# Optimization experiments

Measured on AMD Instinct MI355X. Metric: run time of the kernel, lower is better.

## Reference

```python
import jax, jax.numpy as jnp
import numpy as np

N_NODES = 98304
N_GRAPHS = 2048
NODES_PER_GRAPH = 48
N_EDGES = 393216
NODE_IN = 128
EMB = 64
HID = 256
N_LAYERS = 6
ATTN_DIM = 256
N_HEADS = 4
HEAD_DIM = ATTN_DIM // N_HEADS
OUT_DIM = 1024


def setup_inputs() -> dict:
    key = jax.random.key(0)
    ks = iter(jax.random.split(key, 40))

    def nrm(shape, fan_in):
        return (jax.random.normal(next(ks), shape, dtype=jnp.float32)
                / np.float32(np.sqrt(fan_in)))

    x = jax.random.normal(next(ks), (N_NODES, NODE_IN), dtype=jnp.float32)
    edge_index = jax.random.randint(next(ks), (2, N_EDGES), 0, N_NODES, dtype=jnp.int32)
    batch = (jnp.arange(N_NODES, dtype=jnp.int32) // NODES_PER_GRAPH)

    inp = {
        "x": x,
        "edge_index": edge_index,
        "batch": batch,
        "W_embed": nrm((NODE_IN, EMB), NODE_IN),
        "b_embed": jnp.zeros((EMB,), jnp.float32),
        "W1": nrm((N_LAYERS, EMB, HID), EMB),
        "b1": jnp.zeros((N_LAYERS, HID), jnp.float32),
        "W2": nrm((N_LAYERS, HID, 2 * HID), HID),
        "b2": jnp.zeros((N_LAYERS, 2 * HID), jnp.float32),
        "W3": nrm((N_LAYERS, 2 * HID, EMB), 2 * HID),
        "b3": jnp.zeros((N_LAYERS, EMB), jnp.float32),
        "Wp": nrm((EMB, ATTN_DIM), EMB),
        "bp": jnp.zeros((ATTN_DIM,), jnp.float32),
        "q": jax.random.normal(next(ks), (1, ATTN_DIM), dtype=jnp.float32),
        "W_in": nrm((ATTN_DIM, 3 * ATTN_DIM), ATTN_DIM),
        "b_in": jnp.zeros((3 * ATTN_DIM,), jnp.float32),
        "W_out": nrm((ATTN_DIM, ATTN_DIM), ATTN_DIM),
        "b_out": jnp.zeros((ATTN_DIM,), jnp.float32),
        "Wh1": nrm((ATTN_DIM, HID), ATTN_DIM),
        "bh1": jnp.zeros((HID,), jnp.float32),
        "ln_g": jnp.ones((HID,), jnp.float32),
        "ln_b": jnp.zeros((HID,), jnp.float32),
        "Wh2": nrm((HID, OUT_DIM), HID),
        "bh2": jnp.zeros((OUT_DIM,), jnp.float32),
    }
    return inp


def _forward(x, edge_index, batch, W_embed, b_embed, W1, b1, W2, b2, W3, b3,
             Wp, bp, q, W_in, b_in, W_out, b_out, Wh1, bh1, ln_g, ln_b, Wh2, bh2):
    row = edge_index[0]  # only row is used, matching the torch module

    # node embed
    h = x @ W_embed + b_embed  # [N, 64]

    # 6 GNN layers: gather h[row] -> 3-layer MLP -> scatter_add back to row
    for l in range(N_LAYERS):
        m = jax.nn.relu(h[row] @ W1[l] + b1[l])          # [E, 256]
        m = jax.nn.relu(m @ W2[l] + b2[l])               # [E, 512]
        dh = m @ W3[l] + b3[l]                           # [E, 64]
        h = h + jax.ops.segment_sum(dh, row, num_segments=N_NODES)

    # attention pooling per graph (single learned query, 4 heads)
    hp = h @ Wp + bp                                     # [N, 256]
    Wq, Wk, Wv = W_in[:, :ATTN_DIM], W_in[:, ATTN_DIM:2 * ATTN_DIM], W_in[:, 2 * ATTN_DIM:]
    bq, bk, bv = b_in[:ATTN_DIM], b_in[ATTN_DIM:2 * ATTN_DIM], b_in[2 * ATTN_DIM:]

    qh = ((q @ Wq + bq).reshape(N_HEADS, HEAD_DIM)
          / jnp.asarray(np.sqrt(HEAD_DIM), jnp.float32))  # [H, D]
    k = (hp @ Wk + bk).reshape(N_NODES, N_HEADS, HEAD_DIM)
    v = (hp @ Wv + bv).reshape(N_NODES, N_HEADS, HEAD_DIM)

    scores = jnp.einsum('nhd,hd->nh', k, qh)             # [N, H]
    smax = jax.ops.segment_max(scores, batch, num_segments=N_GRAPHS)  # [B, H]
    e = jnp.exp(scores - smax[batch])
    denom = jax.ops.segment_sum(e, batch, num_segments=N_GRAPHS)      # [B, H]
    w = e / denom[batch]                                  # [N, H]
    pooled = jax.ops.segment_sum(w[:, :, None] * v, batch, num_segments=N_GRAPHS)  # [B, H, D]
    attn = pooled.reshape(N_GRAPHS, ATTN_DIM) @ W_out + b_out  # [B, 256]

    # projection head: ReLU -> Linear -> ReLU -> LayerNorm -> Linear
    t = jax.nn.relu(attn) @ Wh1 + bh1
    t = jax.nn.relu(t)
    mu = jnp.mean(t, axis=-1, keepdims=True)
    var = jnp.mean((t - mu) ** 2, axis=-1, keepdims=True)
    t = (t - mu) * jax.lax.rsqrt(var + 1e-5) * ln_g + ln_b
    return t @ Wh2 + bh2                                  # [B, 1024]


def reference(x, edge_index, batch, W_embed, b_embed, W1, b1, W2, b2, W3, b3,
              Wp, bp, q, W_in, b_in, W_out, b_out, Wh1, bh1, ln_g, ln_b, Wh2, bh2):
    return _forward(x, edge_index, batch, W_embed, b_embed, W1, b1, W2, b2, W3, b3,
                    Wp, bp, q, W_in, b_in, W_out, b_out, Wh1, bh1, ln_g, ln_b, Wh2, bh2)
```

## Files before the change

### kernel.cpp

```cpp
#include <hip/hip_runtime.h>
#include <hip/hip_bf16.h>

#define N_NODES 98304
#define N_GRAPHS 2048
#define N_EDGES 393216
#define EMB 64
#define HID 256
#define N_LAYERS_ 6

typedef __attribute__((ext_vector_type(8))) short short8v;
typedef __attribute__((ext_vector_type(4))) float f32x4;
#define MFMA16(a, b, c) __builtin_amdgcn_mfma_f32_16x16x32_bf16(a, b, c, 0, 0, 0)

__device__ __forceinline__ unsigned short f2bf(float x) {
    unsigned int u = __float_as_uint(x);
    u = (u + 0x7fffu + ((u >> 16) & 1u)) >> 16;
    return (unsigned short)u;
}
__device__ __forceinline__ float bf2f(unsigned short h) {
    return __uint_as_float(((unsigned int)h) << 16);
}
__device__ __forceinline__ int swz(int row, int col, int rowc) {
    return (row * rowc + col) ^ ((row & 7) << 3);
}

__global__ __launch_bounds__(256) void zero_cnt_kernel(int* __restrict__ cnt) {
    int i = blockIdx.x * 256 + threadIdx.x;
    if (i < N_NODES) cnt[i] = 0;
}
__global__ __launch_bounds__(256) void hist_kernel(const int* __restrict__ row,
                                                   int* __restrict__ cnt) {
    int i = blockIdx.x * 256 + threadIdx.x;
    if (i < N_EDGES) atomicAdd(&cnt[row[i]], 1);
}

__global__ __launch_bounds__(64) void prep_frag_kernel(
    const float* __restrict__ W, unsigned short* __restrict__ oh,
    unsigned short* __restrict__ ol, int K, int N)
{
    const int NF = N >> 4, KS = K >> 5;
    const int fpl = NF * KS;
    const int layer = blockIdx.x / fpl;
    const int fid = blockIdx.x % fpl;
    const int nf = fid / KS, ks = fid % KS;
    const int lane = threadIdx.x;
    const float* Wl = W + (size_t)layer * K * N;
    const int n = nf * 16 + (lane & 15);
    const int kb = ks * 32 + (lane >> 4) * 8;
    short8v vh, vl;
    #pragma unroll
    for (int j = 0; j < 8; j++) {
        float wv = Wl[(size_t)(kb + j) * N + n];
        unsigned short hi = f2bf(wv);
        vh[j] = (short)hi;
        vl[j] = (short)f2bf(wv - bf2f(hi));
    }
    size_t o = (size_t)layer * K * N + ((size_t)(nf * KS + ks) * 64 + lane) * 8;
    *reinterpret_cast<short8v*>(oh + o) = vh;
    *reinterpret_cast<short8v*>(ol + o) = vl;
}

__global__ __launch_bounds__(256) void embed_mfma_kernel(
    const float* __restrict__ x,
    const unsigned short* __restrict__ Weh, const unsigned short* __restrict__ Wel,
    const float* __restrict__ b, float* __restrict__ h)
{
    __shared__ __attribute__((aligned(16))) unsigned short xh[32 * 128];
    __shared__ __attribute__((aligned(16))) unsigned short xl[32 * 128];
    const int tid = threadIdx.x;
    const int lane = tid & 63, w = tid >> 6;
    const int lm = lane & 15, lq = lane >> 4;
    const int base = blockIdx.x * 32;
    {
        int row = tid >> 3, c0 = (tid & 7) * 16;
        const float4* p = reinterpret_cast<const float4*>(x + (size_t)(base + row) * 128 + c0);
        float4 u0 = p[0], u1 = p[1], u2 = p[2], u3 = p[3];
        float vals[16] = {u0.x,u0.y,u0.z,u0.w, u1.x,u1.y,u1.z,u1.w,
                          u2.x,u2.y,u2.z,u2.w, u3.x,u3.y,u3.z,u3.w};
        short8v vh0, vl0, vh1, vl1;
        #pragma unroll
        for (int j = 0; j < 8; j++) {
            unsigned short hi = f2bf(vals[j]);
            vh0[j] = (short)hi; vl0[j] = (short)f2bf(vals[j] - bf2f(hi));
            unsigned short hi1 = f2bf(vals[8 + j]);
            vh1[j] = (short)hi1; vl1[j] = (short)f2bf(vals[8 + j] - bf2f(hi1));
        }
        *reinterpret_cast<short8v*>(&xh[swz(row, c0, 128)]) = vh0;
        *reinterpret_cast<short8v*>(&xl[swz(row, c0, 128)]) = vl0;
        *reinterpret_cast<short8v*>(&xh[swz(row, c0 + 8, 128)]) = vh1;
        *reinterpret_cast<short8v*>(&xl[swz(row, c0 + 8, 128)]) = vl1;
    }
    __syncthreads();
    f32x4 acc0, acc1;
    {
        float bv = b[w * 16 + lm];
        acc0 = f32x4{bv, bv, bv, bv};
        acc1 = acc0;
    }
    #pragma unroll
    for (int ks = 0; ks < 4; ks++) {
        short8v a0h = *reinterpret_cast<const short8v*>(&xh[swz(lm, ks * 32 + lq * 8, 128)]);
        short8v a0l = *reinterpret_cast<const short8v*>(&xl[swz(lm, ks * 32 + lq * 8, 128)]);
        short8v a1h = *reinterpret_cast<const short8v*>(&xh[swz(16 + lm, ks * 32 + lq * 8, 128)]);
        short8v a1l = *reinterpret_cast<const short8v*>(&xl[swz(16 + lm, ks * 32 + lq * 8, 128)]);
        size_t bi = ((size_t)(w * 4 + ks) * 64 + lane) * 8;
        short8v bh = *reinterpret_cast<const short8v*>(Weh + bi);
        short8v bl = *reinterpret_cast<const short8v*>(Wel + bi);
        acc0 = MFMA16(a0h, bh, acc0); acc0 = MFMA16(a0l, bh, acc0); acc0 = MFMA16(a0h, bl, acc0);
        acc1 = MFMA16(a1h, bh, acc1); acc1 = MFMA16(a1l, bh, acc1); acc1 = MFMA16(a1h, bl, acc1);
    }
    #pragma unroll
    for (int r = 0; r < 4; r++) {
        h[(size_t)(base + lq * 4 + r) * 64 + w * 16 + lm] = acc0[r];
        h[(size_t)(base + 16 + lq * 4 + r) * 64 + w * 16 + lm] = acc1[r];
    }
}

__global__ __launch_bounds__(512, 4) void layer_mfma_kernel(
    float* __restrict__ h, const int* __restrict__ cnt,
    const unsigned short* __restrict__ W1h, const unsigned short* __restrict__ W1l,
    const float* __restrict__ b1,
    const unsigned short* __restrict__ W2h, const unsigned short* __restrict__ W2l,
    const float* __restrict__ b2,
    const unsigned short* __restrict__ W3h, const unsigned short* __restrict__ W3l,
    const float* __restrict__ b3)
{
    __shared__ __attribute__((aligned(16))) unsigned short hsh[32 * 64];
    __shared__ __attribute__((aligned(16))) unsigned short hsl[32 * 64];
    __shared__ __attribute__((aligned(16))) unsigned short m1h_[32 * 256];
    __shared__ __attribute__((aligned(16))) unsigned short m1l_[32 * 256];
    __shared__ __attribute__((aligned(16))) unsigned short m2h_[32 * 256];
    __shared__ __attribute__((aligned(16))) unsigned short m2l_[32 * 256];
    const int tid = threadIdx.x;
    const int lane = tid & 63, w = tid >> 6;
    const int lm = lane & 15, lq = lane >> 4;
    const int base = blockIdx.x * 32;

    {
        int row = tid >> 4, c0 = (tid & 15) * 4;
        const float4 u = *reinterpret_cast<const float4*>(h + (size_t)(base + row) * 64 + c0);
        float vals[4] = {u.x, u.y, u.z, u.w};
        unsigned short vh[4], vl[4];
        #pragma unroll
        for (int j = 0; j < 4; j++) {
            vh[j] = f2bf(vals[j]);
            vl[j] = f2bf(vals[j] - bf2f(vh[j]));
        }
        int idx = swz(row, c0, 64);
        *reinterpret_cast<uint2*>(&hsh[idx]) = *reinterpret_cast<uint2*>(vh);
        *reinterpret_cast<uint2*>(&hsl[idx]) = *reinterpret_cast<uint2*>(vl);
    }
    __syncthreads();

    {
        f32x4 acc[2][2];
        #pragma unroll
        for (int f = 0; f < 2; f++) {
            float bv = b1[(2 * w + f) * 16 + lm];
            acc[f][0] = f32x4{bv, bv, bv, bv};
            acc[f][1] = acc[f][0];
        }
        #pragma unroll
        for (int ks = 0; ks < 2; ks++) {
            short8v ah0 = *reinterpret_cast<const short8v*>(&hsh[swz(lm, ks * 32 + lq * 8, 64)]);
            short8v al0 = *reinterpret_cast<const short8v*>(&hsl[swz(lm, ks * 32 + lq * 8, 64)]);
            short8v ah1 = *reinterpret_cast<const short8v*>(&hsh[swz(16 + lm, ks * 32 + lq * 8, 64)]);
            short8v al1 = *reinterpret_cast<const short8v*>(&hsl[swz(16 + lm, ks * 32 + lq * 8, 64)]);
            #pragma unroll
            for (int f = 0; f < 2; f++) {
                size_t bi = ((size_t)((2 * w + f) * 2 + ks) * 64 + lane) * 8;
                short8v bh = *reinterpret_cast<const short8v*>(W1h + bi);
                short8v bl = *reinterpret_cast<const short8v*>(W1l + bi);
                acc[f][0] = MFMA16(ah0, bh, acc[f][0]);
                acc[f][0] = MFMA16(al0, bh, acc[f][0]);
                acc[f][0] = MFMA16(ah0, bl, acc[f][0]);
                acc[f][1] = MFMA16(ah1, bh, acc[f][1]);
                acc[f][1] = MFMA16(al1, bh, acc[f][1]);
                acc[f][1] = MFMA16(ah1, bl, acc[f][1]);
            }
        }
        #pragma unroll
        for (int f = 0; f < 2; f++)
            #pragma unroll
            for (int m = 0; m < 2; m++)
                #pragma unroll
                for (int r = 0; r < 4; r++) {
                    int row = m * 16 + lq * 4 + r;
                    int col = (2 * w + f) * 16 + lm;
                    float v = fmaxf(acc[f][m][r], 0.f);
                    unsigned short hi = f2bf(v);
                    m1h_[swz(row, col, 256)] = hi;
                    m1l_[swz(row, col, 256)] = f2bf(v - bf2f(hi));
                }
    }
    __syncthreads();

    const int nfc = w & 3, kq = w >> 2;
    f32x4 dacc[2];
    if (kq == 0) {
        float bv = b3[nfc * 16 + lm];
        dacc[0] = f32x4{bv, bv, bv, bv};
    } else {
        dacc[0] = f32x4{0.f, 0.f, 0.f, 0.f};
    }
    dacc[1] = dacc[0];

    #pragma unroll
    for (int c = 0; c < 2; ++c) {
        {
            f32x4 acc[2][2];
            #pragma unroll
            for (int f = 0; f < 2; f++) {
                float bv = b2[(c * 16 + 2 * w + f) * 16 + lm];
                acc[f][0] = f32x4{bv, bv, bv, bv};
                acc[f][1] = acc[f][0];
            }
            #pragma unroll
            for (int ks = 0; ks < 8; ks++) {
                short8v ah0 = *reinterpret_cast<const short8v*>(&m1h_[swz(lm, ks * 32 + lq * 8, 256)]);
                short8v al0 = *reinterpret_cast<const short8v*>(&m1l_[swz(lm, ks * 32 + lq * 8, 256)]);
                short8v ah1 = *reinterpret_cast<const short8v*>(&m1h_[swz(16 + lm, ks * 32 + lq * 8, 256)]);
                short8v al1 = *reinterpret_cast<const short8v*>(&m1l_[swz(16 + lm, ks * 32 + lq * 8, 256)]);
                #pragma unroll
                for (int f = 0; f < 2; f++) {
                    size_t bi = ((size_t)((c * 16 + 2 * w + f) * 8 + ks) * 64 + lane) * 8;
                    short8v bh = *reinterpret_cast<const short8v*>(W2h + bi);
                    short8v bl = *reinterpret_cast<const short8v*>(W2l + bi);
                    acc[f][0] = MFMA16(ah0, bh, acc[f][0]);
                    acc[f][0] = MFMA16(al0, bh, acc[f][0]);
                    acc[f][0] = MFMA16(ah0, bl, acc[f][0]);
                    acc[f][1] = MFMA16(ah1, bh, acc[f][1]);
                    acc[f][1] = MFMA16(al1, bh, acc[f][1]);
                    acc[f][1] = MFMA16(ah1, bl, acc[f][1]);
                }
            }
            #pragma unroll
            for (int f = 0; f < 2; f++)
                #pragma unroll
                for (int m = 0; m < 2; m++)
                    #pragma unroll
                    for (int r = 0; r < 4; r++) {
                        int row = m * 16 + lq * 4 + r;
                        int col = (2 * w + f) * 16 + lm;
                        float v = fmaxf(acc[f][m][r], 0.f);
                        unsigned short hi = f2bf(v);
                        m2h_[swz(row, col, 256)] = hi;
                        m2l_[swz(row, col, 256)] = f2bf(v - bf2f(hi));
                    }
        }
        __syncthreads();
        {
            #pragma unroll
            for (int kl = 0; kl < 4; kl++) {
                int ksl = kq * 4 + kl;
                short8v ah0 = *reinterpret_cast<const short8v*>(&m2h_[swz(lm, ksl * 32 + lq * 8, 256)]);
                short8v al0 = *reinterpret_cast<const short8v*>(&m2l_[swz(lm, ksl * 32 + lq * 8, 256)]);
                short8v ah1 = *reinterpret_cast<const short8v*>(&m2h_[swz(16 + lm, ksl * 32 + lq * 8, 256)]);
                short8v al1 = *reinterpret_cast<const short8v*>(&m2l_[swz(16 + lm, ksl * 32 + lq * 8, 256)]);
                int ksg = c * 8 + ksl;
                size_t bi = ((size_t)(nfc * 16 + ksg) * 64 + lane) * 8;
                short8v bh = *reinterpret_cast<const short8v*>(W3h + bi);
                short8v bl = *reinterpret_cast<const short8v*>(W3l + bi);
                dacc[0] = MFMA16(ah0, bh, dacc[0]);
                dacc[0] = MFMA16(al0, bh, dacc[0]);
                dacc[0] = MFMA16(ah0, bl, dacc[0]);
                dacc[1] = MFMA16(ah1, bh, dacc[1]);
                dacc[1] = MFMA16(al1, bh, dacc[1]);
                dacc[1] = MFMA16(ah1, bl, dacc[1]);
            }
        }
        __syncthreads();
    }

    float* scr = reinterpret_cast<float*>(m1h_);
    if (kq == 1) {
        #pragma unroll
        for (int m = 0; m < 2; m++)
            #pragma unroll
            for (int r = 0; r < 4; r++)
                scr[(m * 16 + lq * 4 + r) * 64 + nfc * 16 + lm] = dacc[m][r];
    }
    __syncthreads();
    if (kq == 0) {
        #pragma unroll
        for (int m = 0; m < 2; m++)
            #pragma unroll
            for (int r = 0; r < 4; r++) {
                int rr = base + m * 16 + lq * 4 + r;
                float dv = dacc[m][r] + scr[(m * 16 + lq * 4 + r) * 64 + nfc * 16 + lm];
                size_t gi = (size_t)rr * 64 + nfc * 16 + lm;
                h[gi] = h[gi] + (float)cnt[rr] * dv;
            }
    }
}

__global__ __launch_bounds__(256) void prec_kernel(
    const float* __restrict__ q, const float* __restrict__ W_in,
    const float* __restrict__ b_in, const float* __restrict__ Wp,
    const float* __restrict__ bp, float* __restrict__ prec)
{
    __shared__ float qh_s[256];
    __shared__ float u_s[4 * 256];
    const int tid = threadIdx.x;
    {
        float acc = b_in[tid];
        for (int j = 0; j < 256; j++) acc += q[j] * W_in[j * 768 + tid];
        qh_s[tid] = acc * 0.125f;
    }
    __syncthreads();
    {
        #pragma unroll
        for (int hd = 0; hd < 4; hd++) {
            float a = 0.f;
            for (int d = 0; d < 64; d++)
                a += W_in[tid * 768 + 256 + hd * 64 + d] * qh_s[hd * 64 + d];
            u_s[hd * 256 + tid] = a;
        }
    }
    __syncthreads();
    {
        int hd = tid >> 6, i = tid & 63;
        float a = 0.f;
        for (int j = 0; j < 256; j++) a += Wp[i * 256 + j] * u_s[hd * 256 + j];
        prec[hd * 64 + i] = a;
    }
    if (tid < 4) {
        float a = 0.f;
        for (int j = 0; j < 256; j++) a += bp[j] * u_s[tid * 256 + j];
        for (int d = 0; d < 64; d++) a += b_in[256 + tid * 64 + d] * qh_s[tid * 64 + d];
        prec[256 + tid] = a;
    }
}

__global__ __launch_bounds__(64) void attnpool_kernel(
    const float* __restrict__ h, const float* __restrict__ prec,
    float* __restrict__ hw)
{
    __shared__ float hs[48 * 65];
    __shared__ float ss[4 * 64];
    __shared__ float ds_[4];
    __shared__ float wl[48 * 4];
    const int lane = threadIdx.x;
    const int g = blockIdx.x;
    #pragma unroll
    for (int hd = 0; hd < 4; hd++) ss[hd * 64 + lane] = prec[hd * 64 + lane];
    if (lane < 4) ds_[lane] = prec[256 + lane];
    for (int r = 0; r < 48; r++)
        hs[r * 65 + lane] = h[((size_t)g * 48 + r) * 64 + lane];
    __syncthreads();
    float sc[4] = {0.f, 0.f, 0.f, 0.f};
    if (lane < 48) {
        #pragma unroll
        for (int hd = 0; hd < 4; hd++) sc[hd] = ds_[hd];
        for (int c = 0; c < 64; c++) {
            float a = hs[lane * 65 + c];
            #pragma unroll
            for (int hd = 0; hd < 4; hd++) sc[hd] += a * ss[hd * 64 + c];
        }
    }
    #pragma unroll
    for (int hd = 0; hd < 4; hd++) {
        float v = (lane < 48) ? sc[hd] : -3.0e38f;
        #pragma unroll
        for (int m = 32; m >= 1; m >>= 1) v = fmaxf(v, __shfl_xor(v, m, 64));
        float e = (lane < 48) ? __expf(sc[hd] - v) : 0.f;
        float s = e;
        #pragma unroll
        for (int m = 32; m >= 1; m >>= 1) s += __shfl_xor(s, m, 64);
        if (lane < 48) wl[lane * 4 + hd] = e / s;
    }
    __syncthreads();
    float acc[4] = {0.f, 0.f, 0.f, 0.f};
    for (int n = 0; n < 48; n++) {
        float hv = hs[n * 65 + lane];
        #pragma unroll
        for (int hd = 0; hd < 4; hd++) acc[hd] += wl[n * 4 + hd] * hv;
    }
    #pragma unroll
    for (int hd = 0; hd < 4; hd++) hw[(size_t)g * 256 + hd * 64 + lane] = acc[hd];
}

__global__ __launch_bounds__(256) void tail_kernel(
    const float* __restrict__ hw,
    const float* __restrict__ Wp, const float* __restrict__ bp,
    const float* __restrict__ W_in, const float* __restrict__ b_in,
    const float* __restrict__ W_out, const float* __restrict__ b_out,
    const float* __restrict__ Wh1, const float* __restrict__ bh1,
    const float* __restrict__ ln_g, const float* __restrict__ ln_b,
    const float* __restrict__ Wh2, const float* __restrict__ bh2,
    float* __restrict__ out)
{
    __shared__ float hw_s[8 * 256];
    __shared__ float hpw_s[8 * 1024];
    __shared__ float pooled_s[8 * 256];
    __shared__ float attn_s[8 * 256];
    __shared__ float t_s[8 * 256];
    __shared__ float mu_s[8], rs_s[8];
    const int tid = threadIdx.x;
    const int g0 = blockIdx.x * 8;
    #pragma unroll
    for (int r = 0; r < 8; r++)
        hw_s[r * 256 + tid] = hw[(size_t)g0 * 256 + r * 256 + tid];
    __syncthreads();
    {
        float acc[8][4];
        #pragma unroll
        for (int g = 0; g < 8; g++)
            #pragma unroll
            for (int hd = 0; hd < 4; hd++) acc[g][hd] = 0.f;
        for (int i = 0; i < 64; i++) {
            float wv = Wp[i * 256 + tid];
            #pragma unroll
            for (int g = 0; g < 8; g++)
                #pragma unroll
                for (int hd = 0; hd < 4; hd++)
                    acc[g][hd] += hw_s[g * 256 + hd * 64 + i] * wv;
        }
        float bpj = bp[tid];
        #pragma unroll
        for (int g = 0; g < 8; g++)
            #pragma unroll
            for (int hd = 0; hd < 4; hd++)
                hpw_s[g * 1024 + hd * 256 + tid] = acc[g][hd] + bpj;
    }
    __syncthreads();
    {
        const int hd = tid >> 6;
        float acc[8];
        #pragma unroll
        for (int g = 0; g < 8; g++) acc[g] = 0.f;
        for (int j = 0; j < 256; j++) {
            float wv = W_in[j * 768 + 512 + tid];
            #pragma unroll
            for (int g = 0; g < 8; g++)
                acc[g] += hpw_s[g * 1024 + hd * 256 + j] * wv;
        }
        float bb = b_in[512 + tid];
        #pragma unroll
        for (int g = 0; g < 8; g++) pooled_s[g * 256 + tid] = acc[g] + bb;
    }
    __syncthreads();
    {
        float acc[8];
        #pragma unroll
        for (int g = 0; g < 8; g++) acc[g] = 0.f;
        for (int j = 0; j < 256; j++) {
            float wv = W_out[j * 256 + tid];
            #pragma unroll
            for (int g = 0; g < 8; g++) acc[g] += pooled_s[g * 256 + j] * wv;
        }
        float bb = b_out[tid];
        #pragma unroll
        for (int g = 0; g < 8; g++)
            attn_s[g * 256 + tid] = fmaxf(acc[g] + bb, 0.f);
    }
    __syncthreads();
    {
        float acc[8];
        #pragma unroll
        for (int g = 0; g < 8; g++) acc[g] = 0.f;
        for (int j = 0; j < 256; j++) {
            float wv = Wh1[j * 256 + tid];
            #pragma unroll
            for (int g = 0; g < 8; g++) acc[g] += attn_s[g * 256 + j] * wv;
        }
        float bb = bh1[tid];
        #pragma unroll
        for (int g = 0; g < 8; g++)
            t_s[g * 256 + tid] = fmaxf(acc[g] + bb, 0.f);
    }
    __syncthreads();
    if (tid < 8) {
        float s = 0.f;
        for (int c = 0; c < 256; c++) s += t_s[tid * 256 + c];
        float mu = s * (1.f / 256.f);
        float v = 0.f;
        for (int c = 0; c < 256; c++) {
            float d = t_s[tid * 256 + c] - mu;
            v += d * d;
        }
        v *= (1.f / 256.f);
        mu_s[tid] = mu;
        rs_s[tid] = rsqrtf(v + 1e-5f);
    }
    __syncthreads();
    {
        float gg = ln_g[tid], bb = ln_b[tid];
        #pragma unroll
        for (int r = 0; r < 8; r++)
            t_s[r * 256 + tid] = (t_s[r * 256 + tid] - mu_s[r]) * rs_s[r] * gg + bb;
    }
    __syncthreads();
    {
        float acc[8][4];
        float4 bb = *reinterpret_cast<const float4*>(bh2 + tid * 4);
        #pragma unroll
        for (int g = 0; g < 8; g++) {
            acc[g][0] = bb.x; acc[g][1] = bb.y; acc[g][2] = bb.z; acc[g][3] = bb.w;
        }
        for (int j = 0; j < 256; j++) {
            float4 wv = *reinterpret_cast<const float4*>(Wh2 + (size_t)j * 1024 + tid * 4);
            #pragma unroll
            for (int g = 0; g < 8; g++) {
                float tv = t_s[g * 256 + j];
                acc[g][0] += tv * wv.x; acc[g][1] += tv * wv.y;
                acc[g][2] += tv * wv.z; acc[g][3] += tv * wv.w;
            }
        }
        #pragma unroll
        for (int g = 0; g < 8; g++)
            *reinterpret_cast<float4*>(out + (size_t)(g0 + g) * 1024 + tid * 4) =
                make_float4(acc[g][0], acc[g][1], acc[g][2], acc[g][3]);
    }
}

extern "C" void kernel_launch(void* const* d_in, const int* in_sizes, int n_in,
                              void* d_out, int out_size, void* d_ws, size_t ws_size,
                              hipStream_t stream) {
    const float* x       = (const float*)d_in[0];
    const int*   edge    = (const int*)d_in[1];
    const float* W_embed = (const float*)d_in[3];
    const float* b_embed = (const float*)d_in[4];
    const float* W1 = (const float*)d_in[5];
    const float* b1 = (const float*)d_in[6];
    const float* W2 = (const float*)d_in[7];
    const float* b2 = (const float*)d_in[8];
    const float* W3 = (const float*)d_in[9];
    const float* b3 = (const float*)d_in[10];
    const float* Wp = (const float*)d_in[11];
    const float* bp = (const float*)d_in[12];
    const float* q  = (const float*)d_in[13];
    const float* W_in  = (const float*)d_in[14];
    const float* b_in  = (const float*)d_in[15];
    const float* W_out = (const float*)d_in[16];
    const float* b_out = (const float*)d_in[17];
    const float* Wh1 = (const float*)d_in[18];
    const float* bh1 = (const float*)d_in[19];
    const float* ln_g = (const float*)d_in[20];
    const float* ln_b = (const float*)d_in[21];
    const float* Wh2 = (const float*)d_in[22];
    const float* bh2 = (const float*)d_in[23];
    float* out = (float*)d_out;

    char* ws = (char*)d_ws;
    int*   cnt  = (int*)(ws + 0);
    float* h    = (float*)(ws + 393216);
    float* hw   = (float*)(ws + 25559040);
    float* prec = (float*)(ws + 27656192);
    unsigned short* W1h = (unsigned short*)(ws + 27657232);
    unsigned short* W1l = (unsigned short*)(ws + 27853840);
    unsigned short* W2h = (unsigned short*)(ws + 28050448);
    unsigned short* W2l = (unsigned short*)(ws + 29623312);
    unsigned short* W3h = (unsigned short*)(ws + 31196176);
    unsigned short* W3l = (unsigned short*)(ws + 31589392);
    unsigned short* Weh = (unsigned short*)(ws + 31982608);
    unsigned short* Wel = (unsigned short*)(ws + 31998992);

    zero_cnt_kernel<<<N_NODES / 256, 256, 0, stream>>>(cnt);
    hist_kernel<<<N_EDGES / 256, 256, 0, stream>>>(edge, cnt);

    prep_frag_kernel<<<1 * (64 / 16) * (128 / 32), 64, 0, stream>>>(W_embed, Weh, Wel, 128, 64);
    prep_frag_kernel<<<6 * (256 / 16) * (64 / 32), 64, 0, stream>>>(W1, W1h, W1l, 64, 256);
    prep_frag_kernel<<<6 * (512 / 16) * (256 / 32), 64, 0, stream>>>(W2, W2h, W2l, 256, 512);
    prep_frag_kernel<<<6 * (64 / 16) * (512 / 32), 64, 0, stream>>>(W3, W3h, W3l, 512, 64);

    embed_mfma_kernel<<<N_NODES / 32, 256, 0, stream>>>(x, Weh, Wel, b_embed, h);
    for (int l = 0; l < N_LAYERS_; l++) {
        layer_mfma_kernel<<<N_NODES / 32, 512, 0, stream>>>(
            h, cnt,
            W1h + (size_t)l * EMB * HID,     W1l + (size_t)l * EMB * HID,     b1 + (size_t)l * HID,
            W2h + (size_t)l * HID * 2 * HID, W2l + (size_t)l * HID * 2 * HID, b2 + (size_t)l * 2 * HID,
            W3h + (size_t)l * 2 * HID * EMB, W3l + (size_t)l * 2 * HID * EMB, b3 + (size_t)l * EMB);
    }
    prec_kernel<<<1, 256, 0, stream>>>(q, W_in, b_in, Wp, bp, prec);
    attnpool_kernel<<<N_GRAPHS, 64, 0, stream>>>(h, prec, hw);
    tail_kernel<<<N_GRAPHS / 8, 256, 0, stream>>>(hw, Wp, bp, W_in, b_in,
                                                  W_out, b_out, Wh1, bh1,
                                                  ln_g, ln_b, Wh2, bh2, out);
}
```

Measured before the change: 918.7 us.

## Fold Wp into V projection and run tail MLP on split-bf16 MFMA

Precomputes a block-diagonal matrix that folds the Wp projection and the value slice of W_in into one 256x256 operator plus bias, which removes one GEMM stage from the tail. The tail then runs every dense stage (G, W_out, Wh1, Wh2) on 3-pass split-bf16 MFMA over 32-graph tiles, with the intermediates kept in swizzled LDS. LayerNorm is parallelised with shuffle reductions. The cost is extra weight-prep launches and a small change in numerics from the hi/lo bf16 split.

```diff
diff --git a/kernel.cpp b/kernel.cpp
--- a/kernel.cpp
+++ b/kernel.cpp
@@ -58,6 +58,27 @@
     size_t o = (size_t)layer * K * N + ((size_t)(nf * KS + ks) * 64 + lane) * 8;
     *reinterpret_cast<short8v*>(oh + o) = vh;
     *reinterpret_cast<short8v*>(ol + o) = vl;
+}
+
+__global__ __launch_bounds__(256) void gbuild_kernel(
+    const float* __restrict__ Wp, const float* __restrict__ bp,
+    const float* __restrict__ W_in, const float* __restrict__ b_in,
+    float* __restrict__ Gm, float* __restrict__ Gd)
+{
+    const int idx = blockIdx.x * 256 + threadIdx.x;
+    const int q = idx >> 8, p = idx & 255;
+    float s = 0.f;
+    if ((q >> 6) == (p >> 6)) {
+        const float* wr = Wp + (q & 63) * 256;
+        for (int j = 0; j < 256; j++) s += wr[j] * W_in[j * 768 + 512 + p];
+    }
+    Gm[q * 256 + p] = s;
+    if (blockIdx.x == 0) {
+        const int pp = threadIdx.x;
+        float dsum = b_in[512 + pp];
+        for (int j = 0; j < 256; j++) dsum += bp[j] * W_in[j * 768 + 512 + pp];
+        Gd[pp] = dsum;
+    }
 }
 
 __global__ __launch_bounds__(256) void embed_mfma_kernel(
@@ -380,137 +401,173 @@
     for (int hd = 0; hd < 4; hd++) hw[(size_t)g * 256 + hd * 64 + lane] = acc[hd];
 }
 
-__global__ __launch_bounds__(256) void tail_kernel(
+__device__ __forceinline__ void tail_stage(
+    const unsigned short* __restrict__ inh, const unsigned short* __restrict__ inl,
+    const unsigned short* __restrict__ wh, const unsigned short* __restrict__ wl,
+    const float* __restrict__ bias, const bool do_relu,
+    unsigned short* __restrict__ oth, unsigned short* __restrict__ otl,
+    float* __restrict__ tf32,
+    const int w, const int lane, const int lm, const int lq)
+{
+    f32x4 acc[2][2];
+    #pragma unroll
+    for (int f = 0; f < 2; f++) {
+        float bv = bias[(2 * w + f) * 16 + lm];
+        acc[f][0] = f32x4{bv, bv, bv, bv};
+        acc[f][1] = acc[f][0];
+    }
+    #pragma unroll
+    for (int ks = 0; ks < 8; ks++) {
+        short8v ah0 = *reinterpret_cast<const short8v*>(&inh[swz(lm, ks * 32 + lq * 8, 256)]);
+        short8v al0 = *reinterpret_cast<const short8v*>(&inl[swz(lm, ks * 32 + lq * 8, 256)]);
+        short8v ah1 = *reinterpret_cast<const short8v*>(&inh[swz(16 + lm, ks * 32 + lq * 8, 256)]);
+        short8v al1 = *reinterpret_cast<const short8v*>(&inl[swz(16 + lm, ks * 32 + lq * 8, 256)]);
+        #pragma unroll
+        for (int f = 0; f < 2; f++) {
+            size_t bi = ((size_t)((2 * w + f) * 8 + ks) * 64 + lane) * 8;
+            short8v bh = *reinterpret_cast<const short8v*>(wh + bi);
+            short8v bl = *reinterpret_cast<const short8v*>(wl + bi);
+            acc[f][0] = MFMA16(ah0, bh, acc[f][0]);
+            acc[f][0] = MFMA16(al0, bh, acc[f][0]);
+            acc[f][0] = MFMA16(ah0, bl, acc[f][0]);
+            acc[f][1] = MFMA16(ah1, bh, acc[f][1]);
+            acc[f][1] = MFMA16(al1, bh, acc[f][1]);
+            acc[f][1] = MFMA16(ah1, bl, acc[f][1]);
+        }
+    }
+    #pragma unroll
+    for (int f = 0; f < 2; f++)
+        #pragma unroll
+        for (int m = 0; m < 2; m++)
+            #pragma unroll
+            for (int r = 0; r < 4; r++) {
+                int row = m * 16 + lq * 4 + r;
+                int col = (2 * w + f) * 16 + lm;
+                float v = acc[f][m][r];
+                if (do_relu) v = fmaxf(v, 0.f);
+                if (tf32) {
+                    tf32[row * 256 + col] = v;
+                } else {
+                    unsigned short hi = f2bf(v);
+                    oth[swz(row, col, 256)] = hi;
+                    otl[swz(row, col, 256)] = f2bf(v - bf2f(hi));
+                }
+            }
+}
+
+__global__ __launch_bounds__(512, 4) void tail_mfma_kernel(
     const float* __restrict__ hw,
-    const float* __restrict__ Wp, const float* __restrict__ bp,
-    const float* __restrict__ W_in, const float* __restrict__ b_in,
-    const float* __restrict__ W_out, const float* __restrict__ b_out,
-    const float* __restrict__ Wh1, const float* __restrict__ bh1,
+    const unsigned short* __restrict__ Gh, const unsigned short* __restrict__ Gl,
+    const float* __restrict__ Gd,
+    const unsigned short* __restrict__ Woh, const unsigned short* __restrict__ Wol,
+    const float* __restrict__ b_out,
+    const unsigned short* __restrict__ Wh1h, const unsigned short* __restrict__ Wh1l,
+    const float* __restrict__ bh1,
     const float* __restrict__ ln_g, const float* __restrict__ ln_b,
-    const float* __restrict__ Wh2, const float* __restrict__ bh2,
+    const unsigned short* __restrict__ Wh2h, const unsigned short* __restrict__ Wh2l,
+    const float* __restrict__ bh2,
     float* __restrict__ out)
 {
-    __shared__ float hw_s[8 * 256];
-    __shared__ float hpw_s[8 * 1024];
-    __shared__ float pooled_s[8 * 256];
-    __shared__ float attn_s[8 * 256];
-    __shared__ float t_s[8 * 256];
-    __shared__ float mu_s[8], rs_s[8];
+    __shared__ __attribute__((aligned(16))) unsigned short L[32768];
+    unsigned short* Ah = L;
+    unsigned short* Al = L + 8192;
+    unsigned short* Bh = L + 16384;
+    unsigned short* Bl = L + 24576;
+    float* tf = reinterpret_cast<float*>(L + 16384);
     const int tid = threadIdx.x;
-    const int g0 = blockIdx.x * 8;
-    #pragma unroll
-    for (int r = 0; r < 8; r++)
-        hw_s[r * 256 + tid] = hw[(size_t)g0 * 256 + r * 256 + tid];
-    __syncthreads();
-    {
-        float acc[8][4];
-        #pragma unroll
-        for (int g = 0; g < 8; g++)
-            #pragma unroll
-            for (int hd = 0; hd < 4; hd++) acc[g][hd] = 0.f;
-        for (int i = 0; i < 64; i++) {
-            float wv = Wp[i * 256 + tid];
-            #pragma unroll
-            for (int g = 0; g < 8; g++)
-                #pragma unroll
-                for (int hd = 0; hd < 4; hd++)
-                    acc[g][hd] += hw_s[g * 256 + hd * 64 + i] * wv;
-        }
-        float bpj = bp[tid];
-        #pragma unroll
-        for (int g = 0; g < 8; g++)
-            #pragma unroll
-            for (int hd = 0; hd < 4; hd++)
-                hpw_s[g * 1024 + hd * 256 + tid] = acc[g][hd] + bpj;
-    }
-    __syncthreads();
-    {
-        const int hd = tid >> 6;
-        float acc[8];
-        #pragma unroll
-        for (int g = 0; g < 8; g++) acc[g] = 0.f;
-        for (int j = 0; j < 256; j++) {
-            float wv = W_in[j * 768 + 512 + tid];
-            #pragma unroll
-            for (int g = 0; g < 8; g++)
-                acc[g] += hpw_s[g * 1024 + hd * 256 + j] * wv;
-        }
-        float bb = b_in[512 + tid];
-        #pragma unroll
-        for (int g = 0; g < 8; g++) pooled_s[g * 256 + tid] = acc[g] + bb;
-    }
-    __syncthreads();
-    {
-        float acc[8];
-        #pragma unroll
-        for (int g = 0; g < 8; g++) acc[g] = 0.f;
-        for (int j = 0; j < 256; j++) {
-            float wv = W_out[j * 256 + tid];
-            #pragma unroll
-            for (int g = 0; g < 8; g++) acc[g] += pooled_s[g * 256 + j] * wv;
-        }
-        float bb = b_out[tid];
-        #pragma unroll
-        for (int g = 0; g < 8; g++)
-            attn_s[g * 256 + tid] = fmaxf(acc[g] + bb, 0.f);
-    }
-    __syncthreads();
-    {
-        float acc[8];
-        #pragma unroll
-        for (int g = 0; g < 8; g++) acc[g] = 0.f;
-        for (int j = 0; j < 256; j++) {
-            float wv = Wh1[j * 256 + tid];
-            #pragma unroll
-            for (int g = 0; g < 8; g++) acc[g] += attn_s[g * 256 + j] * wv;
-        }
-        float bb = bh1[tid];
-        #pragma unroll
-        for (int g = 0; g < 8; g++)
-            t_s[g * 256 + tid] = fmaxf(acc[g] + bb, 0.f);
-    }
-    __syncthreads();
-    if (tid < 8) {
+    const int lane = tid & 63, w = tid >> 6;
+    const int lm = lane & 15, lq = lane >> 4;
+    const int g0 = blockIdx.x * 32;
+
+    {
+        const float4* hp = reinterpret_cast<const float4*>(hw + (size_t)g0 * 256);
+        #pragma unroll
+        for (int i = 0; i < 4; i++) {
+            int e = tid + 512 * i;
+            int row = e >> 6, c0 = (e & 63) * 4;
+            float4 u = hp[e];
+            float vals[4] = {u.x, u.y, u.z, u.w};
+            unsigned short vh[4], vl[4];
+            #pragma unroll
+            for (int j = 0; j < 4; j++) {
+                vh[j] = f2bf(vals[j]);
+                vl[j] = f2bf(vals[j] - bf2f(vh[j]));
+            }
+            int idx = swz(row, c0, 256);
+            *reinterpret_cast<uint2*>(&Ah[idx]) = *reinterpret_cast<uint2*>(vh);
+            *reinterpret_cast<uint2*>(&Al[idx]) = *reinterpret_cast<uint2*>(vl);
+        }
+    }
+    __syncthreads();
+    tail_stage(Ah, Al, Gh, Gl, Gd, false, Bh, Bl, nullptr, w, lane, lm, lq);
+    __syncthreads();
+    tail_stage(Bh, Bl, Woh, Wol, b_out, true, Ah, Al, nullptr, w, lane, lm, lq);
+    __syncthreads();
+    tail_stage(Ah, Al, Wh1h, Wh1l, bh1, true, nullptr, nullptr, tf, w, lane, lm, lq);
+    __syncthreads();
+    {
+        const int row = tid >> 4, l16 = tid & 15;
         float s = 0.f;
-        for (int c = 0; c < 256; c++) s += t_s[tid * 256 + c];
+        #pragma unroll
+        for (int k = 0; k < 16; k++) s += tf[row * 256 + l16 + 16 * k];
+        #pragma unroll
+        for (int m = 1; m < 16; m <<= 1) s += __shfl_xor(s, m, 16);
         float mu = s * (1.f / 256.f);
         float v = 0.f;
-        for (int c = 0; c < 256; c++) {
-            float d = t_s[tid * 256 + c] - mu;
+        #pragma unroll
+        for (int k = 0; k < 16; k++) {
+            float d = tf[row * 256 + l16 + 16 * k] - mu;
             v += d * d;
         }
-        v *= (1.f / 256.f);
-        mu_s[tid] = mu;
-        rs_s[tid] = rsqrtf(v + 1e-5f);
-    }
-    __syncthreads();
-    {
-        float gg = ln_g[tid], bb = ln_b[tid];
-        #pragma unroll
-        for (int r = 0; r < 8; r++)
-            t_s[r * 256 + tid] = (t_s[r * 256 + tid] - mu_s[r]) * rs_s[r] * gg + bb;
-    }
-    __syncthreads();
-    {
-        float acc[8][4];
-        float4 bb = *reinterpret_cast<const float4*>(bh2 + tid * 4);
-        #pragma unroll
-        for (int g = 0; g < 8; g++) {
-            acc[g][0] = bb.x; acc[g][1] = bb.y; acc[g][2] = bb.z; acc[g][3] = bb.w;
-        }
-        for (int j = 0; j < 256; j++) {
-            float4 wv = *reinterpret_cast<const float4*>(Wh2 + (size_t)j * 1024 + tid * 4);
-            #pragma unroll
-            for (int g = 0; g < 8; g++) {
-                float tv = t_s[g * 256 + j];
-                acc[g][0] += tv * wv.x; acc[g][1] += tv * wv.y;
-                acc[g][2] += tv * wv.z; acc[g][3] += tv * wv.w;
-            }
-        }
-        #pragma unroll
-        for (int g = 0; g < 8; g++)
-            *reinterpret_cast<float4*>(out + (size_t)(g0 + g) * 1024 + tid * 4) =
-                make_float4(acc[g][0], acc[g][1], acc[g][2], acc[g][3]);
+        #pragma unroll
+        for (int m = 1; m < 16; m <<= 1) v += __shfl_xor(v, m, 16);
+        float rs = rsqrtf(v * (1.f / 256.f) + 1e-5f);
+        #pragma unroll
+        for (int k = 0; k < 16; k++) {
+            int col = l16 + 16 * k;
+            float val = (tf[row * 256 + col] - mu) * rs * ln_g[col] + ln_b[col];
+            unsigned short hi = f2bf(val);
+            int idx = swz(row, col, 256);
+            Ah[idx] = hi;
+            Al[idx] = f2bf(val - bf2f(hi));
+        }
+    }
+    __syncthreads();
+    {
+        f32x4 acc[8][2];
+        #pragma unroll
+        for (int f = 0; f < 8; f++) {
+            float bv = bh2[(8 * w + f) * 16 + lm];
+            acc[f][0] = f32x4{bv, bv, bv, bv};
+            acc[f][1] = acc[f][0];
+        }
+        #pragma unroll
+        for (int ks = 0; ks < 8; ks++) {
+            short8v ah0 = *reinterpret_cast<const short8v*>(&Ah[swz(lm, ks * 32 + lq * 8, 256)]);
+            short8v al0 = *reinterpret_cast<const short8v*>(&Al[swz(lm, ks * 32 + lq * 8, 256)]);
+            short8v ah1 = *reinterpret_cast<const short8v*>(&Ah[swz(16 + lm, ks * 32 + lq * 8, 256)]);
+            short8v al1 = *reinterpret_cast<const short8v*>(&Al[swz(16 + lm, ks * 32 + lq * 8, 256)]);
+            #pragma unroll
+            for (int f = 0; f < 8; f++) {
+                size_t bi = ((size_t)((8 * w + f) * 8 + ks) * 64 + lane) * 8;
+                short8v bh = *reinterpret_cast<const short8v*>(Wh2h + bi);
+                short8v bl = *reinterpret_cast<const short8v*>(Wh2l + bi);
+                acc[f][0] = MFMA16(ah0, bh, acc[f][0]);
+                acc[f][0] = MFMA16(al0, bh, acc[f][0]);
+                acc[f][0] = MFMA16(ah0, bl, acc[f][0]);
+                acc[f][1] = MFMA16(ah1, bh, acc[f][1]);
+                acc[f][1] = MFMA16(al1, bh, acc[f][1]);
+                acc[f][1] = MFMA16(ah1, bl, acc[f][1]);
+            }
+        }
+        #pragma unroll
+        for (int f = 0; f < 8; f++)
+            #pragma unroll
+            for (int m = 0; m < 2; m++)
+                #pragma unroll
+                for (int r = 0; r < 4; r++)
+                    out[(size_t)(g0 + m * 16 + lq * 4 + r) * 1024 + (8 * w + f) * 16 + lm]
+                        = acc[f][m][r];
     }
 }
 
@@ -555,6 +612,16 @@
     unsigned short* W3l = (unsigned short*)(ws + 31589392);
     unsigned short* Weh = (unsigned short*)(ws + 31982608);
     unsigned short* Wel = (unsigned short*)(ws + 31998992);
+    float* Gm  = (float*)(ws + 32015376);
+    float* Gd  = (float*)(ws + 32277520);
+    unsigned short* Gfh  = (unsigned short*)(ws + 32278544);
+    unsigned short* Gfl  = (unsigned short*)(ws + 32409616);
+    unsigned short* Wofh = (unsigned short*)(ws + 32540688);
+    unsigned short* Wofl = (unsigned short*)(ws + 32671760);
+    unsigned short* Wh1fh= (unsigned short*)(ws + 32802832);
+    unsigned short* Wh1fl= (unsigned short*)(ws + 32933904);
+    unsigned short* Wh2fh= (unsigned short*)(ws + 33064976);
+    unsigned short* Wh2fl= (unsigned short*)(ws + 33589264);
 
     zero_cnt_kernel<<<N_NODES / 256, 256, 0, stream>>>(cnt);
     hist_kernel<<<N_EDGES / 256, 256, 0, stream>>>(edge, cnt);
@@ -563,6 +630,12 @@
     prep_frag_kernel<<<6 * (256 / 16) * (64 / 32), 64, 0, stream>>>(W1, W1h, W1l, 64, 256);
     prep_frag_kernel<<<6 * (512 / 16) * (256 / 32), 64, 0, stream>>>(W2, W2h, W2l, 256, 512);
     prep_frag_kernel<<<6 * (64 / 16) * (512 / 32), 64, 0, stream>>>(W3, W3h, W3l, 512, 64);
+
+    gbuild_kernel<<<256, 256, 0, stream>>>(Wp, bp, W_in, b_in, Gm, Gd);
+    prep_frag_kernel<<<(256 / 16) * (256 / 32), 64, 0, stream>>>(Gm, Gfh, Gfl, 256, 256);
+    prep_frag_kernel<<<(256 / 16) * (256 / 32), 64, 0, stream>>>(W_out, Wofh, Wofl, 256, 256);
+    prep_frag_kernel<<<(256 / 16) * (256 / 32), 64, 0, stream>>>(Wh1, Wh1fh, Wh1fl, 256, 256);
+    prep_frag_kernel<<<(1024 / 16) * (256 / 32), 64, 0, stream>>>(Wh2, Wh2fh, Wh2fl, 256, 1024);
 
     embed_mfma_kernel<<<N_NODES / 32, 256, 0, stream>>>(x, Weh, Wel, b_embed, h);
     for (int l = 0; l < N_LAYERS_; l++) {
@@ -574,7 +647,7 @@
     }
     prec_kernel<<<1, 256, 0, stream>>>(q, W_in, b_in, Wp, bp, prec);
     attnpool_kernel<<<N_GRAPHS, 64, 0, stream>>>(h, prec, hw);
-    tail_kernel<<<N_GRAPHS / 8, 256, 0, stream>>>(hw, Wp, bp, W_in, b_in,
-                                                  W_out, b_out, Wh1, bh1,
-                                                  ln_g, ln_b, Wh2, bh2, out);
-}
+    tail_mfma_kernel<<<N_GRAPHS / 32, 512, 0, stream>>>(
+        hw, Gfh, Gfl, Gd, Wofh, Wofl, b_out, Wh1fh, Wh1fl, bh1,
+        ln_g, ln_b, Wh2fh, Wh2fl, bh2, out);
+}
```

Measured after the change: 882.2 us. 4.0% less time.
